# Kernel tuning notes

Hardware: AMD Instinct MI355X
Metric: run time of the kernel (lower is better)

## Reference

```python
import jax, jax.numpy as jnp
import numpy as np

N = 50000      # nodes
E = 600000     # edges
C = 128        # in_channels
H = 128        # hidden_channels
O = 128        # out_channels
G = 512        # graphs in batch
BN_EPS = 1e-5


def setup_inputs() -> dict:
    key = jax.random.key(0)
    ks = jax.random.split(key, 16)

    def w(k, shape):
        return jax.random.normal(k, shape, dtype=jnp.float32) * 0.05

    inp = {}
    inp["x"] = jax.random.normal(ks[0], (N, C), dtype=jnp.float32)
    inp["edge_index"] = jax.random.randint(ks[1], (2, E), 0, N, dtype=jnp.int64)
    inp["batch"] = jnp.sort(jax.random.randint(ks[2], (N,), 0, G, dtype=jnp.int64))

    dims = [(C, H, H), (H, H, H), (H, H, O)]
    ki = 3
    for li, (din, dh, dout) in enumerate(dims, 1):
        inp[f"g{li}_W1"] = w(ks[ki], (din, dh)); inp[f"g{li}_b1"] = jnp.zeros((dh,), jnp.float32)
        inp[f"g{li}_gm"] = jnp.ones((dh,), jnp.float32); inp[f"g{li}_bt"] = jnp.zeros((dh,), jnp.float32)
        inp[f"g{li}_rm"] = jnp.zeros((dh,), jnp.float32); inp[f"g{li}_rv"] = jnp.ones((dh,), jnp.float32)
        inp[f"g{li}_W2"] = w(ks[ki + 1], (dh, dout)); inp[f"g{li}_b2"] = jnp.zeros((dout,), jnp.float32)
        ki += 2
    inp["lin_W"] = w(ks[ki], (H + H + O, O))
    inp["lin_b"] = jnp.zeros((O,), jnp.float32)
    return inp


def gin_conv(x, src, dst, W1, b1, gm, bt, rm, rv, W2, b2):
    # GINConv (eps=0): mlp(x + sum_{j in N(i)} x_j); mlp = Linear-BN(eval)-ReLU-Linear
    agg = jax.ops.segment_sum(x[src], dst, num_segments=N)   # [N, d] scatter-add
    h = (x + agg) @ W1 + b1
    h = (h - rm) * jax.lax.rsqrt(rv + BN_EPS) * gm + bt      # BatchNorm1d, eval mode
    return jax.nn.relu(h) @ W2 + b2


def reference(x, edge_index, batch,
              g1_W1, g1_b1, g1_gm, g1_bt, g1_rm, g1_rv, g1_W2, g1_b2,
              g2_W1, g2_b1, g2_gm, g2_bt, g2_rm, g2_rv, g2_W2, g2_b2,
              g3_W1, g3_b1, g3_gm, g3_bt, g3_rm, g3_rv, g3_W2, g3_b2,
              lin_W, lin_b):
    src, dst = edge_index[0], edge_index[1]
    # dropout(0.2) is identity in eval mode
    x1 = jax.nn.relu(gin_conv(x, src, dst, g1_W1, g1_b1, g1_gm, g1_bt, g1_rm, g1_rv, g1_W2, g1_b2))
    x2 = jax.nn.relu(gin_conv(x1, src, dst, g2_W1, g2_b1, g2_gm, g2_bt, g2_rm, g2_rv, g2_W2, g2_b2))
    x3 = gin_conv(x2, src, dst, g3_W1, g3_b1, g3_gm, g3_bt, g3_rm, g3_rv, g3_W2, g3_b2)
    xc = jnp.concatenate([x1, x2, x3], axis=-1)              # JumpingKnowledge 'cat' -> [N, H+H+O]
    sums = jax.ops.segment_sum(xc, batch, num_segments=G)    # global_mean_pool
    cnt = jax.ops.segment_sum(jnp.ones((N, 1), xc.dtype), batch, num_segments=G)
    pooled = sums / jnp.maximum(cnt, 1.0)                    # [G, H+H+O]
    return pooled @ lin_W + lin_b                            # [G, O]
```

## Files before the change

### kernel.cpp

```cpp
#include <hip/hip_runtime.h>
#include <hip/hip_bf16.h>

#define NNODES 50000
#define NEDGES 600000
#define NGRAPHS 512
#define BN_EPS 1e-5f

typedef short bf16x8 __attribute__((ext_vector_type(8)));
typedef float f32x4 __attribute__((ext_vector_type(4)));

__device__ __forceinline__ void bf_split(float x, ushort& h, ushort& l) {
    __hip_bfloat16 bh = __float2bfloat16(x);
    float r = x - __bfloat162float(bh);
    __hip_bfloat16 bl = __float2bfloat16(r);
    h = __builtin_bit_cast(ushort, bh);
    l = __builtin_bit_cast(ushort, bl);
}
__device__ __forceinline__ ushort f2b(float x) {
    return __builtin_bit_cast(ushort, __float2bfloat16(x));
}
__device__ __forceinline__ float b2f(ushort u) {
    union { uint i; float f; } c; c.i = ((uint)u) << 16; return c.f;
}

__global__ __launch_bounds__(256) void prep_kernel(
    const float* __restrict__ x, ushort* __restrict__ xh,
    float* __restrict__ pooled, int* __restrict__ counts, int* __restrict__ row_ptr,
    const float* W0, const float* W1, const float* W2, const float* W3,
    const float* W4, const float* W5, ushort* __restrict__ hi, ushort* __restrict__ lo) {
    int b = blockIdx.x, t = threadIdx.x;
    if (b < 3125) {
        int f4 = b * 512 + t * 2;
        float4 a0 = ((const float4*)x)[f4];
        float4 a1 = ((const float4*)x)[f4 + 1];
        ushort4 u0 = {f2b(a0.x), f2b(a0.y), f2b(a0.z), f2b(a0.w)};
        ushort4 u1 = {f2b(a1.x), f2b(a1.y), f2b(a1.z), f2b(a1.w)};
        int e0 = f4 * 4;
        *(ushort4*)(xh + e0) = u0;
        *(ushort4*)(xh + e0 + 4) = u1;
        if (b == 0 && t == 0) row_ptr[NNODES] = NEDGES;
    } else if (b < 3317) {
        ((float4*)pooled)[(b - 3125) * 256 + t] = make_float4(0.f, 0.f, 0.f, 0.f);
    } else if (b < 3513) {
        int i = (b - 3317) * 256 + t;
        if (i < NNODES) counts[i] = 0;
    } else {
        int wb = b - 3513;
        const float* Ws[6] = {W0, W1, W2, W3, W4, W5};
        const float* W = Ws[wb >> 4];
        ushort* h = hi + (size_t)(wb >> 4) * 16384;
        ushort* l = lo + (size_t)(wb >> 4) * 16384;
        int chunk = wb & 15;
#pragma unroll
        for (int i = 0; i < 4; i++) {
            int idx = chunk * 1024 + i * 256 + t;
            int n = idx >> 7, k = idx & 127;
            ushort hh, ll;
            bf_split(W[k * 128 + n], hh, ll);
            h[n * 128 + k] = hh;
            l[n * 128 + k] = ll;
        }
    }
}

__global__ __launch_bounds__(256) void hist_kernel(const int* __restrict__ dst,
                                                   int* __restrict__ counts, int E) {
    int i = blockIdx.x * 256 + threadIdx.x;
    if (i < E) atomicAdd(&counts[dst[i]], 1);
}

__global__ __launch_bounds__(256) void scan1_kernel(const int* __restrict__ counts,
                                                    int* __restrict__ partials, int n) {
    __shared__ int s[256];
    int i = blockIdx.x * 256 + threadIdx.x;
    int v = (i < n) ? counts[i] : 0;
    s[threadIdx.x] = v;
    __syncthreads();
    for (int off = 128; off > 0; off >>= 1) {
        if (threadIdx.x < off) s[threadIdx.x] += s[threadIdx.x + off];
        __syncthreads();
    }
    if (threadIdx.x == 0) partials[blockIdx.x] = s[0];
}

__global__ __launch_bounds__(256) void scan3_kernel(const int* __restrict__ counts,
                                                    const int* __restrict__ partials,
                                                    int* __restrict__ row_ptr,
                                                    int* __restrict__ cursor, int n, int nb) {
    __shared__ int s[256];
    __shared__ int base_sh;
    int t = threadIdx.x;
    int pv = (t < (int)blockIdx.x && t < nb) ? partials[t] : 0;
    s[t] = pv;
    __syncthreads();
    for (int off = 128; off > 0; off >>= 1) {
        if (t < off) s[t] += s[t + off];
        __syncthreads();
    }
    if (t == 0) base_sh = s[0];
    __syncthreads();
    int base = base_sh;
    int i = blockIdx.x * 256 + t;
    int v = (i < n) ? counts[i] : 0;
    __syncthreads();
    s[t] = v;
    __syncthreads();
    for (int off = 1; off < 256; off <<= 1) {
        int nv = (t >= off) ? s[t - off] : 0;
        __syncthreads();
        s[t] += nv;
        __syncthreads();
    }
    if (i < n) {
        int ex = base + s[t] - v;
        row_ptr[i] = ex;
        cursor[i] = ex;
    }
}

__global__ __launch_bounds__(256) void scatter_kernel(const int* __restrict__ src,
                                                      const int* __restrict__ dst,
                                                      int* __restrict__ cursor,
                                                      int* __restrict__ esrc, int E) {
    int i = blockIdx.x * 256 + threadIdx.x;
    if (i < E) {
        int p = atomicAdd(&cursor[dst[i]], 1);
        esrc[p] = src[i];
    }
}

template <bool SELF_F32>
__global__ __launch_bounds__(256) void agg_kernel(
    const float* __restrict__ xf, const ushort* __restrict__ phi,
    const int* __restrict__ rp, const int* __restrict__ esrc,
    ushort* __restrict__ ohi, int n) {
    int wid  = (blockIdx.x * 256 + threadIdx.x) >> 6;
    int lane = threadIdx.x & 63;
    int node = wid * 2 + (lane >> 5);
    int q = lane & 31;
    if (node >= n) return;
    const ushort4* xh = (const ushort4*)phi;
    float4 acc;
    if (SELF_F32) {
        acc = ((const float4*)xf)[(size_t)node * 32 + q];
    } else {
        ushort4 sh = xh[(size_t)node * 32 + q];
        acc.x = b2f(sh.x); acc.y = b2f(sh.y); acc.z = b2f(sh.z); acc.w = b2f(sh.w);
    }
    int beg = rp[node], end = rp[node + 1];
    int e = beg;
    for (; e + 8 <= end; e += 8) {
        int i0 = esrc[e],     i1 = esrc[e + 1], i2 = esrc[e + 2], i3 = esrc[e + 3];
        int i4 = esrc[e + 4], i5 = esrc[e + 5], i6 = esrc[e + 6], i7 = esrc[e + 7];
        ushort4 v0 = xh[(size_t)i0 * 32 + q];
        ushort4 v1 = xh[(size_t)i1 * 32 + q];
        ushort4 v2 = xh[(size_t)i2 * 32 + q];
        ushort4 v3 = xh[(size_t)i3 * 32 + q];
        ushort4 v4 = xh[(size_t)i4 * 32 + q];
        ushort4 v5 = xh[(size_t)i5 * 32 + q];
        ushort4 v6 = xh[(size_t)i6 * 32 + q];
        ushort4 v7 = xh[(size_t)i7 * 32 + q];
        acc.x += ((b2f(v0.x) + b2f(v1.x)) + (b2f(v2.x) + b2f(v3.x))) +
                 ((b2f(v4.x) + b2f(v5.x)) + (b2f(v6.x) + b2f(v7.x)));
        acc.y += ((b2f(v0.y) + b2f(v1.y)) + (b2f(v2.y) + b2f(v3.y))) +
                 ((b2f(v4.y) + b2f(v5.y)) + (b2f(v6.y) + b2f(v7.y)));
        acc.z += ((b2f(v0.z) + b2f(v1.z)) + (b2f(v2.z) + b2f(v3.z))) +
                 ((b2f(v4.z) + b2f(v5.z)) + (b2f(v6.z) + b2f(v7.z)));
        acc.w += ((b2f(v0.w) + b2f(v1.w)) + (b2f(v2.w) + b2f(v3.w))) +
                 ((b2f(v4.w) + b2f(v5.w)) + (b2f(v6.w) + b2f(v7.w)));
    }
    for (; e + 2 <= end; e += 2) {
        int i0 = esrc[e], i1 = esrc[e + 1];
        ushort4 v0 = xh[(size_t)i0 * 32 + q];
        ushort4 v1 = xh[(size_t)i1 * 32 + q];
        acc.x += b2f(v0.x) + b2f(v1.x); acc.y += b2f(v0.y) + b2f(v1.y);
        acc.z += b2f(v0.z) + b2f(v1.z); acc.w += b2f(v0.w) + b2f(v1.w);
    }
    for (; e < end; e++) {
        ushort4 v = xh[(size_t)esrc[e] * 32 + q];
        acc.x += b2f(v.x); acc.y += b2f(v.y); acc.z += b2f(v.z); acc.w += b2f(v.w);
    }
    ushort4 hh = {f2b(acc.x), f2b(acc.y), f2b(acc.z), f2b(acc.w)};
    *(ushort4*)(ohi + (size_t)node * 128 + q * 4) = hh;
}

template <bool RELU_OUT, bool WRITE_PLANES>
__global__ __launch_bounds__(256) void mlp_kernel(
    const ushort* __restrict__ Ah,
    const ushort* __restrict__ W1hi, const ushort* __restrict__ W1lo,
    const ushort* __restrict__ W2hi, const ushort* __restrict__ W2lo,
    const float* __restrict__ b1, const float* __restrict__ gm,
    const float* __restrict__ bt, const float* __restrict__ rm,
    const float* __restrict__ rv, const float* __restrict__ b2,
    ushort* __restrict__ Ch,
    const int* __restrict__ batch, float* __restrict__ pooled, int poff, int M) {
    __shared__ __align__(16) ushort smem[128 * 136];
    __shared__ int bsm[128];
    const int t = threadIdx.x;
    const int lane = t & 63;
    const int wv = t >> 6;
    const int wr = wv >> 1, wc = wv & 1;
    const int row0 = blockIdx.x * 128;
    const int g = lane >> 4, c = lane & 15;

    if (t < 128) bsm[t] = (row0 + t < M) ? batch[row0 + t] : -1;

    const int m0 = t >> 2,  k80 = (t & 3) * 8;
    const int m1 = m0 + 64;
    int r0 = row0 + m0; if (r0 >= M) r0 = M - 1;
    int r1 = row0 + m1; if (r1 >= M) r1 = M - 1;
    const size_t ga0 = (size_t)r0 * 128 + k80;
    const size_t ga1 = (size_t)r1 * 128 + k80;
    const int la0 = m0 * 32 + k80, la1 = m1 * 32 + k80;

    f32x4 acc[4][4];
#pragma unroll
    for (int i = 0; i < 4; i++)
#pragma unroll
        for (int j = 0; j < 4; j++) acc[i][j] = (f32x4){0.f, 0.f, 0.f, 0.f};

    uint4 ph0 = *(const uint4*)(Ah + ga0);
    uint4 ph1 = *(const uint4*)(Ah + ga1);
    *(uint4*)&smem[la0] = ph0;
    *(uint4*)&smem[la1] = ph1;
    __syncthreads();

    int cur = 0;
    for (int kb = 0; kb < 4; kb++) {
        bf16x8 bh[4], bl[4];
#pragma unroll
        for (int ct = 0; ct < 4; ct++) {
            const size_t wo = (size_t)(wc * 64 + ct * 16 + c) * 128 + kb * 32 + g * 8;
            bh[ct] = *(const bf16x8*)(W1hi + wo);
            bl[ct] = *(const bf16x8*)(W1lo + wo);
        }
        if (kb < 3) {
            const size_t o = (size_t)(kb + 1) * 32;
            ph0 = *(const uint4*)(Ah + ga0 + o);
            ph1 = *(const uint4*)(Ah + ga1 + o);
        }
        bf16x8 ah[4];
#pragma unroll
        for (int rt = 0; rt < 4; rt++) {
            int off = cur * 4096 + (wr * 64 + rt * 16 + c) * 32 + g * 8;
            ah[rt] = *(bf16x8*)&smem[off];
        }
#pragma unroll
        for (int rt = 0; rt < 4; rt++)
#pragma unroll
            for (int ct = 0; ct < 4; ct++) {
                acc[rt][ct] = __builtin_amdgcn_mfma_f32_16x16x32_bf16(ah[rt], bh[ct], acc[rt][ct], 0, 0, 0);
                acc[rt][ct] = __builtin_amdgcn_mfma_f32_16x16x32_bf16(ah[rt], bl[ct], acc[rt][ct], 0, 0, 0);
            }
        if (kb < 3) {
            *(uint4*)&smem[(cur ^ 1) * 4096 + la0] = ph0;
            *(uint4*)&smem[(cur ^ 1) * 4096 + la1] = ph1;
        }
        __syncthreads();
        cur ^= 1;
    }

    {
        float cs[4], ca[4];
#pragma unroll
        for (int ct = 0; ct < 4; ct++) {
            int n = wc * 64 + ct * 16 + c;
            float s = gm[n] * rsqrtf(rv[n] + BN_EPS);
            cs[ct] = s;
            ca[ct] = (b1[n] - rm[n]) * s + bt[n];
        }
#pragma unroll
        for (int rt = 0; rt < 4; rt++)
#pragma unroll
            for (int r = 0; r < 4; r++) {
                int row = wr * 64 + rt * 16 + g * 4 + r;
#pragma unroll
                for (int ct = 0; ct < 4; ct++) {
                    int col = wc * 64 + ct * 16 + c;
                    float v = fmaxf(acc[rt][ct][r] * cs[ct] + ca[ct], 0.f);
                    smem[row * 136 + col] = f2b(v);
                }
            }
    }
    __syncthreads();

#pragma unroll
    for (int i = 0; i < 4; i++)
#pragma unroll
        for (int j = 0; j < 4; j++) acc[i][j] = (f32x4){0.f, 0.f, 0.f, 0.f};

    for (int kb = 0; kb < 4; kb++) {
        bf16x8 bh[4], bl[4];
#pragma unroll
        for (int ct = 0; ct < 4; ct++) {
            const size_t wo = (size_t)(wc * 64 + ct * 16 + c) * 128 + kb * 32 + g * 8;
            bh[ct] = *(const bf16x8*)(W2hi + wo);
            bl[ct] = *(const bf16x8*)(W2lo + wo);
        }
        bf16x8 ah[4];
#pragma unroll
        for (int rt = 0; rt < 4; rt++) {
            int off = (wr * 64 + rt * 16 + c) * 136 + kb * 32 + g * 8;
            ah[rt] = *(bf16x8*)&smem[off];
        }
#pragma unroll
        for (int rt = 0; rt < 4; rt++)
#pragma unroll
            for (int ct = 0; ct < 4; ct++) {
                acc[rt][ct] = __builtin_amdgcn_mfma_f32_16x16x32_bf16(ah[rt], bh[ct], acc[rt][ct], 0, 0, 0);
                acc[rt][ct] = __builtin_amdgcn_mfma_f32_16x16x32_bf16(ah[rt], bl[ct], acc[rt][ct], 0, 0, 0);
            }
    }
    __syncthreads();

    {
        float ca2[4];
#pragma unroll
        for (int ct = 0; ct < 4; ct++) ca2[ct] = b2[wc * 64 + ct * 16 + c];
#pragma unroll
        for (int rt = 0; rt < 4; rt++)
#pragma unroll
            for (int r = 0; r < 4; r++) {
                int rl = wr * 64 + rt * 16 + g * 4 + r;
                int row = row0 + rl;
                bool valid = row < M;
#pragma unroll
                for (int ct = 0; ct < 4; ct++) {
                    int col = wc * 64 + ct * 16 + c;
                    float v = acc[rt][ct][r] + ca2[ct];
                    if (RELU_OUT) v = fmaxf(v, 0.f);
                    ushort hh = f2b(valid ? v : 0.f);
                    smem[rl * 136 + col] = hh;
                    if (WRITE_PLANES && valid) Ch[(size_t)row * 128 + col] = hh;
                }
            }
    }
    __syncthreads();

    {
        int col = t & 127;
        int rbase = (t >> 7) * 64;
        int gcur = bsm[rbase];
        float accp = 0.f;
#pragma unroll 8
        for (int r = 0; r < 64; r++) {
            int gg = bsm[rbase + r];
            if (gg != gcur) {
                if (gcur >= 0) atomicAdd(&pooled[gcur * 384 + poff + col], accp);
                accp = 0.f;
                gcur = gg;
            }
            accp += b2f(smem[(rbase + r) * 136 + col]);
        }
        if (gcur >= 0) atomicAdd(&pooled[gcur * 384 + poff + col], accp);
    }
}

__global__ __launch_bounds__(128) void final_kernel(const float* __restrict__ pooled,
                                                    const int* __restrict__ batch,
                                                    const float* __restrict__ W,
                                                    const float* __restrict__ b,
                                                    float* __restrict__ out, int n) {
    __shared__ float ps[384];
    int gph = blockIdx.x, t = threadIdx.x;
    int lo1 = 0, hi1 = n;
    while (lo1 < hi1) { int mid = (lo1 + hi1) >> 1; if (batch[mid] < gph) lo1 = mid + 1; else hi1 = mid; }
    int start = lo1;
    int lo2 = start, hi2 = n;
    while (lo2 < hi2) { int mid = (lo2 + hi2) >> 1; if (batch[mid] < gph + 1) lo2 = mid + 1; else hi2 = mid; }
    int cnt = lo2 - start;
    float inv = 1.f / (float)(cnt > 0 ? cnt : 1);
    for (int i = t; i < 384; i += 128) ps[i] = pooled[gph * 384 + i] * inv;
    __syncthreads();
    float acc = b[t];
#pragma unroll 8
    for (int k = 0; k < 384; k++) acc += ps[k] * W[k * 128 + t];
    out[gph * 128 + t] = acc;
}

extern "C" void kernel_launch(void* const* d_in, const int* in_sizes, int n_in,
                              void* d_out, int out_size, void* d_ws, size_t ws_size,
                              hipStream_t stream) {
    const float* x     = (const float*)d_in[0];
    const int*   edge  = (const int*)d_in[1];
    const int*   batch = (const int*)d_in[2];
    const float* p[32];
    for (int i = 0; i < n_in && i < 32; i++) p[i] = (const float*)d_in[i];
    const float* lin_W = p[27];
    const float* lin_b = p[28];

    char* w = (char*)d_ws;
    auto alloc = [&](size_t bytes) { void* r = (void*)w; w += (bytes + 255) & ~(size_t)255; return r; };
    const size_t PL = (size_t)NNODES * 128;
    ushort* thi   = (ushort*)alloc(PL * 2);
    ushort* xh0   = (ushort*)alloc(PL * 2);
    ushort* p1h   = (ushort*)alloc(PL * 2);
    ushort* p2h   = xh0;
    float* pooled = (float*)alloc((size_t)NGRAPHS * 384 * 4);
    int* counts   = (int*)alloc((size_t)NNODES * 4);
    int* cursor   = (int*)alloc((size_t)NNODES * 4);
    int* row_ptr  = (int*)alloc((size_t)(NNODES + 1) * 4);
    int* esrc     = (int*)alloc((size_t)NEDGES * 4);
    int* partials = (int*)alloc(256 * 4);
    ushort* wt_hi = (ushort*)alloc((size_t)6 * 16384 * 2);
    ushort* wt_lo = (ushort*)alloc((size_t)6 * 16384 * 2);

    const int* src = edge;
    const int* dst = edge + NEDGES;

    prep_kernel<<<3609, 256, 0, stream>>>(x, xh0, pooled, counts, row_ptr,
                                          p[3], p[9], p[11], p[17], p[19], p[25],
                                          wt_hi, wt_lo);

    int nb = (NNODES + 255) / 256;
    hist_kernel<<<(NEDGES + 255) / 256, 256, 0, stream>>>(dst, counts, NEDGES);
    scan1_kernel<<<nb, 256, 0, stream>>>(counts, partials, NNODES);
    scan3_kernel<<<nb, 256, 0, stream>>>(counts, partials, row_ptr, cursor, NNODES, nb);
    scatter_kernel<<<(NEDGES + 255) / 256, 256, 0, stream>>>(src, dst, cursor, esrc, NEDGES);

    int mlp_grid = (NNODES + 127) / 128;
    int agg_grid = (NNODES / 2 * 64 + 255) / 256;

    agg_kernel<true><<<agg_grid, 256, 0, stream>>>(x, xh0, row_ptr, esrc, thi, NNODES);
    mlp_kernel<true, true><<<mlp_grid, 256, 0, stream>>>(thi,
        wt_hi + 0 * 16384, wt_lo + 0 * 16384, wt_hi + 1 * 16384, wt_lo + 1 * 16384,
        p[4], p[5], p[6], p[7], p[8], p[10], p1h, batch, pooled, 0, NNODES);
    agg_kernel<false><<<agg_grid, 256, 0, stream>>>(nullptr, p1h, row_ptr, esrc, thi, NNODES);
    mlp_kernel<true, true><<<mlp_grid, 256, 0, stream>>>(thi,
        wt_hi + 2 * 16384, wt_lo + 2 * 16384, wt_hi + 3 * 16384, wt_lo + 3 * 16384,
        p[12], p[13], p[14], p[15], p[16], p[18], p2h, batch, pooled, 128, NNODES);
    agg_kernel<false><<<agg_grid, 256, 0, stream>>>(nullptr, p2h, row_ptr, esrc, thi, NNODES);
    mlp_kernel<false, false><<<mlp_grid, 256, 0, stream>>>(thi,
        wt_hi + 4 * 16384, wt_lo + 4 * 16384, wt_hi + 5 * 16384, wt_lo + 5 * 16384,
        p[20], p[21], p[22], p[23], p[24], p[26], nullptr, batch, pooled, 256, NNODES);

    final_kernel<<<NGRAPHS, 128, 0, stream>>>(pooled, batch, lin_W, lin_b,
                                              (float*)d_out, NNODES);
}
```

Before: 365.9 us.

## Shrink MLP tiles to 64 rows with two waves; use bf16 self term in first aggregation

The MLP kernel moves from 128-row tiles with four waves in a 2x2 layout to 64-row tiles with two waves, each wave covering all 64 rows and half the columns. This doubles the grid, roughly halves shared memory per block, and is meant to raise occupancy and improve load balance. The first aggregation now reads the self term from the bf16 copy of x instead of the fp32 input, which cuts load traffic but slightly reduces precision. Each weight fragment is now reused over fewer rows, so total weight loads per node rise. The A-tile load offsets (m1 = m0+32) and the smem double-buffer stride (4096) look consistent with the new 64-row tile.

New measurement: 363.8 us. No clear change (-0.6%).

```diff
diff --git a/kernel.cpp b/kernel.cpp
--- a/kernel.cpp
+++ b/kernel.cpp
@@ -129,9 +129,8 @@
     }
 }
 
-template <bool SELF_F32>
 __global__ __launch_bounds__(256) void agg_kernel(
-    const float* __restrict__ xf, const ushort* __restrict__ phi,
+    const ushort* __restrict__ phi,
     const int* __restrict__ rp, const int* __restrict__ esrc,
     ushort* __restrict__ ohi, int n) {
     int wid  = (blockIdx.x * 256 + threadIdx.x) >> 6;
@@ -140,13 +139,9 @@
     int q = lane & 31;
     if (node >= n) return;
     const ushort4* xh = (const ushort4*)phi;
+    ushort4 sh = xh[(size_t)node * 32 + q];
     float4 acc;
-    if (SELF_F32) {
-        acc = ((const float4*)xf)[(size_t)node * 32 + q];
-    } else {
-        ushort4 sh = xh[(size_t)node * 32 + q];
-        acc.x = b2f(sh.x); acc.y = b2f(sh.y); acc.z = b2f(sh.z); acc.w = b2f(sh.w);
-    }
+    acc.x = b2f(sh.x); acc.y = b2f(sh.y); acc.z = b2f(sh.z); acc.w = b2f(sh.w);
     int beg = rp[node], end = rp[node + 1];
     int e = beg;
     for (; e + 8 <= end; e += 8) {
@@ -185,7 +180,7 @@
 }
 
 template <bool RELU_OUT, bool WRITE_PLANES>
-__global__ __launch_bounds__(256) void mlp_kernel(
+__global__ __launch_bounds__(128) void mlp_kernel(
     const ushort* __restrict__ Ah,
     const ushort* __restrict__ W1hi, const ushort* __restrict__ W1lo,
     const ushort* __restrict__ W2hi, const ushort* __restrict__ W2lo,
@@ -194,19 +189,18 @@
     const float* __restrict__ rv, const float* __restrict__ b2,
     ushort* __restrict__ Ch,
     const int* __restrict__ batch, float* __restrict__ pooled, int poff, int M) {
-    __shared__ __align__(16) ushort smem[128 * 136];
-    __shared__ int bsm[128];
+    __shared__ __align__(16) ushort smem[64 * 136];
+    __shared__ int bsm[64];
     const int t = threadIdx.x;
     const int lane = t & 63;
     const int wv = t >> 6;
-    const int wr = wv >> 1, wc = wv & 1;
-    const int row0 = blockIdx.x * 128;
+    const int row0 = blockIdx.x * 64;
     const int g = lane >> 4, c = lane & 15;
 
-    if (t < 128) bsm[t] = (row0 + t < M) ? batch[row0 + t] : -1;
-
-    const int m0 = t >> 2,  k80 = (t & 3) * 8;
-    const int m1 = m0 + 64;
+    if (t < 64) bsm[t] = (row0 + t < M) ? batch[row0 + t] : -1;
+
+    const int m0 = t >> 2, k80 = (t & 3) * 8;
+    const int m1 = m0 + 32;
     int r0 = row0 + m0; if (r0 >= M) r0 = M - 1;
     int r1 = row0 + m1; if (r1 >= M) r1 = M - 1;
     const size_t ga0 = (size_t)r0 * 128 + k80;
@@ -230,7 +224,7 @@
         bf16x8 bh[4], bl[4];
 #pragma unroll
         for (int ct = 0; ct < 4; ct++) {
-            const size_t wo = (size_t)(wc * 64 + ct * 16 + c) * 128 + kb * 32 + g * 8;
+            const size_t wo = (size_t)(wv * 64 + ct * 16 + c) * 128 + kb * 32 + g * 8;
             bh[ct] = *(const bf16x8*)(W1hi + wo);
             bl[ct] = *(const bf16x8*)(W1lo + wo);
         }
@@ -242,7 +236,7 @@
         bf16x8 ah[4];
 #pragma unroll
         for (int rt = 0; rt < 4; rt++) {
-            int off = cur * 4096 + (wr * 64 + rt * 16 + c) * 32 + g * 8;
+            int off = cur * 4096 + (rt * 16 + c) * 32 + g * 8;
             ah[rt] = *(bf16x8*)&smem[off];
         }
 #pragma unroll
@@ -264,7 +258,7 @@
         float cs[4], ca[4];
 #pragma unroll
         for (int ct = 0; ct < 4; ct++) {
-            int n = wc * 64 + ct * 16 + c;
+            int n = wv * 64 + ct * 16 + c;
             float s = gm[n] * rsqrtf(rv[n] + BN_EPS);
             cs[ct] = s;
             ca[ct] = (b1[n] - rm[n]) * s + bt[n];
@@ -273,10 +267,10 @@
         for (int rt = 0; rt < 4; rt++)
 #pragma unroll
             for (int r = 0; r < 4; r++) {
-                int row = wr * 64 + rt * 16 + g * 4 + r;
+                int row = rt * 16 + g * 4 + r;
 #pragma unroll
                 for (int ct = 0; ct < 4; ct++) {
-                    int col = wc * 64 + ct * 16 + c;
+                    int col = wv * 64 + ct * 16 + c;
                     float v = fmaxf(acc[rt][ct][r] * cs[ct] + ca[ct], 0.f);
                     smem[row * 136 + col] = f2b(v);
                 }
@@ -293,14 +287,14 @@
         bf16x8 bh[4], bl[4];
 #pragma unroll
         for (int ct = 0; ct < 4; ct++) {
-            const size_t wo = (size_t)(wc * 64 + ct * 16 + c) * 128 + kb * 32 + g * 8;
+            const size_t wo = (size_t)(wv * 64 + ct * 16 + c) * 128 + kb * 32 + g * 8;
             bh[ct] = *(const bf16x8*)(W2hi + wo);
             bl[ct] = *(const bf16x8*)(W2lo + wo);
         }
         bf16x8 ah[4];
 #pragma unroll
         for (int rt = 0; rt < 4; rt++) {
-            int off = (wr * 64 + rt * 16 + c) * 136 + kb * 32 + g * 8;
+            int off = (rt * 16 + c) * 136 + kb * 32 + g * 8;
             ah[rt] = *(bf16x8*)&smem[off];
         }
 #pragma unroll
@@ -316,17 +310,17 @@
     {
         float ca2[4];
 #pragma unroll
-        for (int ct = 0; ct < 4; ct++) ca2[ct] = b2[wc * 64 + ct * 16 + c];
+        for (int ct = 0; ct < 4; ct++) ca2[ct] = b2[wv * 64 + ct * 16 + c];
 #pragma unroll
         for (int rt = 0; rt < 4; rt++)
 #pragma unroll
             for (int r = 0; r < 4; r++) {
-                int rl = wr * 64 + rt * 16 + g * 4 + r;
+                int rl = rt * 16 + g * 4 + r;
                 int row = row0 + rl;
                 bool valid = row < M;
 #pragma unroll
                 for (int ct = 0; ct < 4; ct++) {
-                    int col = wc * 64 + ct * 16 + c;
+                    int col = wv * 64 + ct * 16 + c;
                     float v = acc[rt][ct][r] + ca2[ct];
                     if (RELU_OUT) v = fmaxf(v, 0.f);
                     ushort hh = f2b(valid ? v : 0.f);
@@ -338,19 +332,18 @@
     __syncthreads();
 
     {
-        int col = t & 127;
-        int rbase = (t >> 7) * 64;
-        int gcur = bsm[rbase];
+        int col = t;
+        int gcur = bsm[0];
         float accp = 0.f;
 #pragma unroll 8
         for (int r = 0; r < 64; r++) {
-            int gg = bsm[rbase + r];
+            int gg = bsm[r];
             if (gg != gcur) {
                 if (gcur >= 0) atomicAdd(&pooled[gcur * 384 + poff + col], accp);
                 accp = 0.f;
                 gcur = gg;
             }
-            accp += b2f(smem[(rbase + r) * 136 + col]);
+            accp += b2f(smem[r * 136 + col]);
         }
         if (gcur >= 0) atomicAdd(&pooled[gcur * 384 + poff + col], accp);
     }
@@ -418,19 +411,19 @@
     scan3_kernel<<<nb, 256, 0, stream>>>(counts, partials, row_ptr, cursor, NNODES, nb);
     scatter_kernel<<<(NEDGES + 255) / 256, 256, 0, stream>>>(src, dst, cursor, esrc, NEDGES);
 
-    int mlp_grid = (NNODES + 127) / 128;
+    int mlp_grid = (NNODES + 63) / 64;
     int agg_grid = (NNODES / 2 * 64 + 255) / 256;
 
-    agg_kernel<true><<<agg_grid, 256, 0, stream>>>(x, xh0, row_ptr, esrc, thi, NNODES);
-    mlp_kernel<true, true><<<mlp_grid, 256, 0, stream>>>(thi,
+    agg_kernel<<<agg_grid, 256, 0, stream>>>(xh0, row_ptr, esrc, thi, NNODES);
+    mlp_kernel<true, true><<<mlp_grid, 128, 0, stream>>>(thi,
         wt_hi + 0 * 16384, wt_lo + 0 * 16384, wt_hi + 1 * 16384, wt_lo + 1 * 16384,
         p[4], p[5], p[6], p[7], p[8], p[10], p1h, batch, pooled, 0, NNODES);
-    agg_kernel<false><<<agg_grid, 256, 0, stream>>>(nullptr, p1h, row_ptr, esrc, thi, NNODES);
-    mlp_kernel<true, true><<<mlp_grid, 256, 0, stream>>>(thi,
+    agg_kernel<<<agg_grid, 256, 0, stream>>>(p1h, row_ptr, esrc, thi, NNODES);
+    mlp_kernel<true, true><<<mlp_grid, 128, 0, stream>>>(thi,
         wt_hi + 2 * 16384, wt_lo + 2 * 16384, wt_hi + 3 * 16384, wt_lo + 3 * 16384,
         p[12], p[13], p[14], p[15], p[16], p[18], p2h, batch, pooled, 128, NNODES);
-    agg_kernel<false><<<agg_grid, 256, 0, stream>>>(nullptr, p2h, row_ptr, esrc, thi, NNODES);
-    mlp_kernel<false, false><<<mlp_grid, 256, 0, stream>>>(thi,
+    agg_kernel<<<agg_grid, 256, 0, stream>>>(p2h, row_ptr, esrc, thi, NNODES);
+    mlp_kernel<false, false><<<mlp_grid, 128, 0, stream>>>(thi,
         wt_hi + 4 * 16384, wt_lo + 4 * 16384, wt_hi + 5 * 16384, wt_lo + 5 * 16384,
         p[20], p[21], p[22], p[23], p[24], p[26], nullptr, batch, pooled, 256, NNODES);
 
```
